# Kernel tuning notes

Hardware: AMD Instinct MI355X
Metric: run time of the kernel (lower is better)

The kernel has to match this reference:

```python
import jax, jax.numpy as jnp
import numpy as np

N, C = 131072, 32          # scene points, raw feature channels
K, L, B1 = 2048, 64, 8     # points per leaf, num leaves, level-1 branching
D_PROJ, D_HID, D = 128, 256, 512


def _lin(key, fan_in, fan_out):
    return jax.random.normal(key, (fan_in, fan_out), jnp.float32) / np.sqrt(fan_in)


def setup_inputs() -> dict:
    key = jax.random.key(0)
    ks = jax.random.split(key, 12)
    coords = jax.random.normal(ks[0], (N, 3), jnp.float32)
    feats = jax.random.normal(ks[1], (N, C), jnp.float32)
    # regular partition of the scene into 64 leaves of 2048 points each
    leaf_indices = jnp.arange(N, dtype=jnp.int32).reshape(L, K)
    leaf_center_idx = jax.random.randint(ks[2], (L,), 0, N, dtype=jnp.int32)
    l1_center_idx = jax.random.randint(ks[3], (B1,), 0, N, dtype=jnp.int32)
    return {
        'coords': coords, 'feats': feats,
        'leaf_indices': leaf_indices,
        'leaf_center_idx': leaf_center_idx,
        'l1_center_idx': l1_center_idx,
        'root_center_idx': 0,
        # projection MLP: C -> 128 -> 128
        'Wp1': _lin(ks[4], C, D_PROJ), 'bp1': jnp.zeros((D_PROJ,), jnp.float32),
        'Wp2': _lin(ks[5], D_PROJ, D_PROJ), 'bp2': jnp.zeros((D_PROJ,), jnp.float32),
        # encoder per-point MLP: (3 + 128) -> 256 -> 512
        'We1': _lin(ks[6], 3 + D_PROJ, D_HID), 'be1': jnp.zeros((D_HID,), jnp.float32),
        'We2': _lin(ks[7], D_HID, D), 'be2': jnp.zeros((D,), jnp.float32),
        # aggregator: (D + 3) -> 512 per child, max-pool, 512 -> 512
        'Wa1': _lin(ks[8], D + 3, D), 'ba1': jnp.zeros((D,), jnp.float32),
        'Wa2': _lin(ks[9], D, D), 'ba2': jnp.zeros((D,), jnp.float32),
    }


def reference(coords, feats, leaf_indices, leaf_center_idx, l1_center_idx,
              root_center_idx, Wp1, bp1, Wp2, bp2, We1, be1, We2, be2,
              Wa1, ba1, Wa2, ba2):
    # ---- leaves: gather + projection + PointNet encoder (batched over all leaves) ----
    pts = coords[leaf_indices]                       # (L, K, 3)
    pf = feats[leaf_indices]                         # (L, K, C)
    centers = coords[leaf_center_idx]                # (L, 3)
    rel = pts - centers[:, None, :]                  # relative coords
    proj = jax.nn.relu(pf @ Wp1 + bp1) @ Wp2 + bp2   # (L, K, D_PROJ)
    x = jnp.concatenate([rel, proj], axis=-1)        # (L, K, 3+D_PROJ)
    h = jax.nn.relu(x @ We1 + be1)                   # (L, K, D_HID)
    point_feats = jax.nn.relu(h @ We2 + be2)         # (L, K, D)
    leaf_feat = point_feats.max(axis=1)              # (L, D) max pool per leaf

    # ---- aggregator with spatial context ----
    def aggregate(child_feats, child_pos, parent_pos):
        r = child_pos - parent_pos[None, :]                       # (M, 3)
        z = jnp.concatenate([child_feats, r], axis=-1)            # (M, D+3)
        g = jax.nn.relu(z @ Wa1 + ba1)                            # (M, D)
        return g.max(axis=0) @ Wa2 + ba2                          # (D,)

    # level 1: each of B1 parents aggregates L//B1 leaf children
    cf = leaf_feat.reshape(B1, L // B1, D)
    cp = centers.reshape(B1, L // B1, 3)
    pp = coords[l1_center_idx]                                    # (B1, 3)
    level1 = jax.vmap(aggregate)(cf, cp, pp)                      # (B1, D)

    # level 0: root aggregates the B1 level-1 features
    root = aggregate(level1, pp, coords[root_center_idx])         # (D,)

    # rows: [level_0 (1), level_1 (B1), level_2 (L)]
    return jnp.concatenate([root[None, :], level1, leaf_feat], axis=0)
```

## Files before the change

### kernel.cpp

```cpp
#include <hip/hip_runtime.h>

#define NPTS   131072
#define CIN    32
#define KPL    2048
#define NLEAF  64
#define NB1    8
#define DPJ    128
#define DHID   256
#define DOUT   512
#define TM     128

typedef __attribute__((ext_vector_type(8))) short  short8;
typedef __attribute__((ext_vector_type(4))) float  f32x4;

__device__ __forceinline__ unsigned short f2bf(float x) {
    unsigned u = __float_as_uint(x);
    u += 0x7FFFu + ((u >> 16) & 1u);
    return (unsigned short)(u >> 16);
}

__global__ __launch_bounds__(256) void prep_weights(
    const float* __restrict__ Wp1, const float* __restrict__ We2,
    const float* __restrict__ Wp2, const float* __restrict__ We1,
    const float* __restrict__ bp2, const float* __restrict__ be1,
    unsigned short* __restrict__ wp1t, unsigned short* __restrict__ we2t,
    unsigned short* __restrict__ wft, float* __restrict__ bfused)
{
    const int b = blockIdx.x;
    if (b < 528) {
        int idx = b * 256 + threadIdx.x;
        if (idx < 4096) {
            int n = idx / 32, k = idx % 32;
            wp1t[idx] = f2bf(Wp1[k * DPJ + n]);
        } else if (idx < 4096 + 131072) {
            int i = idx - 4096;
            int n = i / 256, k = i % 256;
            we2t[i] = f2bf(We2[k * DOUT + n]);
        }
    } else if (b < 656) {
        const int k = b - 528;
        const int n = threadIdx.x;
        float a0 = 0.f, a1 = 0.f, a2 = 0.f, a3 = 0.f;
        #pragma unroll
        for (int j = 0; j < DPJ; j += 4) {
            a0 += Wp2[k * DPJ + j    ] * We1[(3 + j) * DHID + n];
            a1 += Wp2[k * DPJ + j + 1] * We1[(4 + j) * DHID + n];
            a2 += Wp2[k * DPJ + j + 2] * We1[(5 + j) * DHID + n];
            a3 += Wp2[k * DPJ + j + 3] * We1[(6 + j) * DHID + n];
        }
        wft[n * DPJ + k] = f2bf((a0 + a1) + (a2 + a3));
    } else {
        const int n = threadIdx.x;
        float s0 = be1[n], s1 = 0.f, s2 = 0.f, s3 = 0.f;
        #pragma unroll
        for (int j = 0; j < DPJ; j += 4) {
            s0 += bp2[j    ] * We1[(3 + j) * DHID + n];
            s1 += bp2[j + 1] * We1[(4 + j) * DHID + n];
            s2 += bp2[j + 2] * We1[(5 + j) * DHID + n];
            s3 += bp2[j + 3] * We1[(6 + j) * DHID + n];
        }
        bfused[n] = (s0 + s1) + (s2 + s3);
    }
}

template<int MF, int NF, int KSTEPS, int SB, int WK>
__device__ __forceinline__ void gemm_core(
    const char* sIn, const unsigned short* __restrict__ wt,
    const float* __restrict__ bias, int cb, int lr, int lg, f32x4 acc[MF][NF])
{
    #pragma unroll
    for (int n = 0; n < NF; ++n) {
        float bv = bias[cb + 16 * n + lr];
        #pragma unroll
        for (int m = 0; m < MF; ++m) acc[m][n] = f32x4{bv, bv, bv, bv};
    }
    #pragma unroll
    for (int kk = 0; kk < KSTEPS; ++kk) {
        short8 b[NF];
        #pragma unroll
        for (int n = 0; n < NF; ++n)
            b[n] = *reinterpret_cast<const short8*>(
                wt + (size_t)(cb + 16 * n + lr) * WK + kk * 32 + lg * 8);
        #pragma unroll
        for (int m = 0; m < MF; ++m) {
            int row  = 16 * m + lr;
            int byte = (row * SB + kk * 64 + lg * 16) ^ ((row & 7) << 4);
            short8 a = *reinterpret_cast<const short8*>(sIn + byte);
            #pragma unroll
            for (int n = 0; n < NF; ++n)
                acc[m][n] = __builtin_amdgcn_mfma_f32_16x16x32_bf16(a, b[n], acc[m][n], 0, 0, 0);
        }
    }
}

template<int MF, int NF, int SB, bool RELU>
__device__ __forceinline__ void store_frag(char* sOut, int cb, int lr, int lg, f32x4 acc[MF][NF])
{
    #pragma unroll
    for (int m = 0; m < MF; ++m) {
        #pragma unroll
        for (int r = 0; r < 4; ++r) {
            int row = 16 * m + lg * 4 + r;
            int rb  = row * SB;
            int sw  = (row & 7) << 4;
            #pragma unroll
            for (int n = 0; n < NF; ++n) {
                float v = acc[m][n][r];
                if (RELU) v = fmaxf(v, 0.f);
                int byte = (rb + (cb + 16 * n + lr) * 2) ^ sw;
                *reinterpret_cast<unsigned short*>(sOut + byte) = f2bf(v);
            }
        }
    }
}

template<int MF, int NF>
__device__ __forceinline__ void pool_frag(float* dst, int cb, int lr, int lg, f32x4 acc[MF][NF])
{
    #pragma unroll
    for (int n = 0; n < NF; ++n) {
        float vm = 0.f;
        #pragma unroll
        for (int m = 0; m < MF; ++m) {
            #pragma unroll
            for (int r = 0; r < 4; ++r) vm = fmaxf(vm, acc[m][n][r]);
        }
        vm = fmaxf(vm, __shfl_xor(vm, 16));
        vm = fmaxf(vm, __shfl_xor(vm, 32));
        if (lg == 0)
            atomicMax(reinterpret_cast<int*>(dst + cb + 16 * n + lr),
                      __float_as_int(vm));
    }
}

__global__ __launch_bounds__(256, 1) void leaf_mfma_kernel(
    const float* __restrict__ coords, const float* __restrict__ feats,
    const int* __restrict__ leaf_indices, const int* __restrict__ leaf_center_idx,
    const unsigned short* __restrict__ wp1t, const float* __restrict__ bp1,
    const unsigned short* __restrict__ wft, const float* __restrict__ bfused,
    const float* __restrict__ We1raw,
    const unsigned short* __restrict__ we2t, const float* __restrict__ be2,
    float* __restrict__ leaf_out)
{
    __shared__ __align__(16) char buf[96 * 1024];
    __shared__ float s_rel[TM][4];
    __shared__ float s_we1rel[3 * DHID];

    const int t    = threadIdx.x;
    const int lane = t & 63;
    const int w    = t >> 6;
    const int lr   = lane & 15;
    const int lg   = lane >> 4;

    const int l     = blockIdx.x >> 4;
    const int chunk = blockIdx.x & 15;
    const int base  = l * KPL + chunk * TM;

    char* const sX  = buf;
    char* const sH  = buf;
    char* const sP1 = buf + 65536;

    {
        const int p  = t >> 1;
        const int kq = (t & 1) << 4;
        const int gi = leaf_indices[base + p];
        const float* src = feats + (size_t)gi * CIN + kq;
        float4 v0 = *reinterpret_cast<const float4*>(src);
        float4 v1 = *reinterpret_cast<const float4*>(src + 4);
        float4 v2 = *reinterpret_cast<const float4*>(src + 8);
        float4 v3 = *reinterpret_cast<const float4*>(src + 12);
        short8 o0, o1;
        o0[0] = (short)f2bf(v0.x); o0[1] = (short)f2bf(v0.y);
        o0[2] = (short)f2bf(v0.z); o0[3] = (short)f2bf(v0.w);
        o0[4] = (short)f2bf(v1.x); o0[5] = (short)f2bf(v1.y);
        o0[6] = (short)f2bf(v1.z); o0[7] = (short)f2bf(v1.w);
        o1[0] = (short)f2bf(v2.x); o1[1] = (short)f2bf(v2.y);
        o1[2] = (short)f2bf(v2.z); o1[3] = (short)f2bf(v2.w);
        o1[4] = (short)f2bf(v3.x); o1[5] = (short)f2bf(v3.y);
        o1[6] = (short)f2bf(v3.z); o1[7] = (short)f2bf(v3.w);
        const int sw = (p & 7) << 4;
        int b0 = (p * (CIN * 2) + kq * 2) ^ sw;
        int b1 = (p * (CIN * 2) + kq * 2 + 16) ^ sw;
        *reinterpret_cast<short8*>(sX + b0) = o0;
        *reinterpret_cast<short8*>(sX + b1) = o1;
    }
    if (t < TM) {
        const int gi = leaf_indices[base + t];
        const int ci = leaf_center_idx[l];
        s_rel[t][0] = coords[gi * 3 + 0] - coords[ci * 3 + 0];
        s_rel[t][1] = coords[gi * 3 + 1] - coords[ci * 3 + 1];
        s_rel[t][2] = coords[gi * 3 + 2] - coords[ci * 3 + 2];
    }
    #pragma unroll
    for (int j = 0; j < 3; ++j) s_we1rel[j * DHID + t] = We1raw[j * DHID + t];
    __syncthreads();

    {
        f32x4 acc[8][2];
        gemm_core<8, 2, 1, CIN * 2, 32>(sX, wp1t, bp1, w * 32, lr, lg, acc);
        store_frag<8, 2, DPJ * 2, true>(sP1, w * 32, lr, lg, acc);
    }
    __syncthreads();

    {
        const int cb = w * 64;
        f32x4 acc[8][4];
        gemm_core<8, 4, 4, DPJ * 2, DPJ>(sP1, wft, bfused, cb, lr, lg, acc);
        #pragma unroll
        for (int m = 0; m < 8; ++m) {
            #pragma unroll
            for (int r = 0; r < 4; ++r) {
                int row = 16 * m + lg * 4 + r;
                float r0 = s_rel[row][0], r1 = s_rel[row][1], r2 = s_rel[row][2];
                #pragma unroll
                for (int n = 0; n < 4; ++n) {
                    int col = cb + 16 * n + lr;
                    acc[m][n][r] += r0 * s_we1rel[col]
                                  + r1 * s_we1rel[DHID + col]
                                  + r2 * s_we1rel[2 * DHID + col];
                }
            }
        }
        store_frag<8, 4, DHID * 2, true>(sH, cb, lr, lg, acc);
    }
    __syncthreads();

    {
        float* const dst = leaf_out + (size_t)l * DOUT;
        #pragma unroll
        for (int p4 = 0; p4 < 2; ++p4) {
            const int cb = w * 128 + p4 * 64;
            f32x4 acc[8][4];
            gemm_core<8, 4, 8, DHID * 2, 256>(sH, we2t, be2, cb, lr, lg, acc);
            pool_frag<8, 4>(dst, cb, lr, lg, acc);
        }
    }
}

__global__ __launch_bounds__(256) void agg_pool_kernel(
    const float* __restrict__ child,
    const float* __restrict__ coords,
    const int* __restrict__ child_idx,
    const int* __restrict__ parent_idx,
    const float* __restrict__ Wa1, const float* __restrict__ ba1,
    float* __restrict__ pooled)
{
    __shared__ float s_z[NB1][516];
    __shared__ float s_red[4][NB1][64];

    const int t  = threadIdx.x;
    const int b  = blockIdx.x;
    const int p  = b >> 3, cc = b & 7;
    const int c  = t & 63;
    const int col = cc * 64 + c;
    const int ks = t >> 6;

    {
        const int m = t >> 5, tt = t & 31;
        const float* src = child + (size_t)(p * NB1 + m) * DOUT;
        #pragma unroll
        for (int i = 0; i < 4; ++i) {
            const int idx = (i * 32 + tt) * 4;
            *reinterpret_cast<float4*>(&s_z[m][idx]) =
                *reinterpret_cast<const float4*>(src + idx);
        }
    }
    if (t < 24) {
        const int m = t / 3, j = t % 3;
        s_z[m][512 + j] = coords[child_idx[p * NB1 + m] * 3 + j]
                        - coords[parent_idx[p] * 3 + j];
    }
    __syncthreads();

    float acc[NB1] = {0.f, 0.f, 0.f, 0.f, 0.f, 0.f, 0.f, 0.f};
    const int k0 = ks * 128;
    #pragma unroll 32
    for (int i = 0; i < 128; ++i) {
        const int k = k0 + i;
        const float wv = Wa1[(size_t)k * DOUT + col];
        #pragma unroll
        for (int m = 0; m < NB1; ++m) acc[m] += s_z[m][k] * wv;
    }
    if (ks == 3) {
        #pragma unroll
        for (int k = 512; k < 515; ++k) {
            const float wv = Wa1[(size_t)k * DOUT + col];
            #pragma unroll
            for (int m = 0; m < NB1; ++m) acc[m] += s_z[m][k] * wv;
        }
    }
    #pragma unroll
    for (int m = 0; m < NB1; ++m) s_red[ks][m][c] = acc[m];
    __syncthreads();

    if (t < 64) {
        const float bv = ba1[col];
        float pm = 0.f;
        #pragma unroll
        for (int m = 0; m < NB1; ++m) {
            float v = bv + s_red[0][m][c] + s_red[1][m][c]
                         + s_red[2][m][c] + s_red[3][m][c];
            pm = fmaxf(pm, v);
        }
        pooled[(size_t)p * DOUT + col] = pm;
    }
}

__global__ __launch_bounds__(256) void agg_out_kernel(
    const float* __restrict__ pooled,
    const float* __restrict__ Wa2, const float* __restrict__ ba2,
    float* __restrict__ outbase)
{
    __shared__ float s_p[DOUT];
    __shared__ float s_red[4][64];

    const int t  = threadIdx.x;
    const int b  = blockIdx.x;
    const int p  = b >> 3, cc = b & 7;
    const int c  = t & 63;
    const int col = cc * 64 + c;
    const int ks = t >> 6;

    if (t < 128)
        *reinterpret_cast<float4*>(&s_p[t * 4]) =
            *reinterpret_cast<const float4*>(pooled + (size_t)p * DOUT + t * 4);
    __syncthreads();

    float acc = 0.f;
    const int k0 = ks * 128;
    #pragma unroll 32
    for (int i = 0; i < 128; ++i) {
        const int k = k0 + i;
        acc += s_p[k] * Wa2[(size_t)k * DOUT + col];
    }
    s_red[ks][c] = acc;
    __syncthreads();

    if (t < 64)
        outbase[(size_t)p * DOUT + col] =
            ba2[col] + s_red[0][c] + s_red[1][c] + s_red[2][c] + s_red[3][c];
}

extern "C" void kernel_launch(void* const* d_in, const int* in_sizes, int n_in,
                              void* d_out, int out_size, void* d_ws, size_t ws_size,
                              hipStream_t stream)
{
    const float* coords          = (const float*)d_in[0];
    const float* feats           = (const float*)d_in[1];
    const int*   leaf_indices    = (const int*)d_in[2];
    const int*   leaf_center_idx = (const int*)d_in[3];
    const int*   l1_center_idx   = (const int*)d_in[4];
    const int*   root_center_idx = (const int*)d_in[5];
    const float* Wp1 = (const float*)d_in[6];
    const float* bp1 = (const float*)d_in[7];
    const float* Wp2 = (const float*)d_in[8];
    const float* bp2 = (const float*)d_in[9];
    const float* We1 = (const float*)d_in[10];
    const float* be1 = (const float*)d_in[11];
    const float* We2 = (const float*)d_in[12];
    const float* be2 = (const float*)d_in[13];
    const float* Wa1 = (const float*)d_in[14];
    const float* ba1 = (const float*)d_in[15];
    const float* Wa2 = (const float*)d_in[16];
    const float* ba2 = (const float*)d_in[17];

    float* out = (float*)d_out;
    char*  ws  = (char*)d_ws;
    unsigned short* wp1t     = (unsigned short*)ws;
    unsigned short* we2t     = (unsigned short*)(ws + 8192);
    unsigned short* wft      = (unsigned short*)(ws + 270336);
    float*          bfused   = (float*)(ws + 335872);
    float*          pooledL1 = (float*)(ws + 336896);
    float*          pooledR  = (float*)(ws + 353280);

    hipMemsetAsync(out + (size_t)(1 + NB1) * DOUT, 0,
                   (size_t)NLEAF * DOUT * sizeof(float), stream);

    prep_weights<<<dim3(657), dim3(256), 0, stream>>>(
        Wp1, We2, Wp2, We1, bp2, be1, wp1t, we2t, wft, bfused);

    leaf_mfma_kernel<<<dim3(NLEAF * (KPL / TM)), dim3(256), 0, stream>>>(
        coords, feats, leaf_indices, leaf_center_idx,
        wp1t, bp1, wft, bfused, We1, we2t, be2,
        out + (size_t)(1 + NB1) * DOUT);

    agg_pool_kernel<<<dim3(NB1 * 8), dim3(256), 0, stream>>>(
        out + (size_t)(1 + NB1) * DOUT, coords, leaf_center_idx, l1_center_idx,
        Wa1, ba1, pooledL1);
    agg_out_kernel<<<dim3(NB1 * 8), dim3(256), 0, stream>>>(
        pooledL1, Wa2, ba2, out + DOUT);

    agg_pool_kernel<<<dim3(8), dim3(256), 0, stream>>>(
        out + DOUT, coords, l1_center_idx, root_center_idx,
        Wa1, ba1, pooledR);
    agg_out_kernel<<<dim3(8), dim3(256), 0, stream>>>(
        pooledR, Wa2, ba2, out);
}
```

Measured before the change: 114.2 us.

## Fuse aggregator levels into one kernel with atomic-counter inter-block dependencies

Replaces the four small aggregator launches with a single 144-block kernel. Blocks wait on global atomic counters (spin-wait with s_sleep) for their producer stage before running, and read cross-block data through atomic loads to bypass stale caches. The leaf-row memset and counter reset are folded into extra blocks of the weight-prep kernel. This removes several launch gaps and one memset call, but relies on all 144 blocks being co-resident and adds spin-wait and atomic-read overhead.

```diff
diff --git a/kernel.cpp b/kernel.cpp
--- a/kernel.cpp
+++ b/kernel.cpp
@@ -24,7 +24,8 @@
     const float* __restrict__ Wp2, const float* __restrict__ We1,
     const float* __restrict__ bp2, const float* __restrict__ be1,
     unsigned short* __restrict__ wp1t, unsigned short* __restrict__ we2t,
-    unsigned short* __restrict__ wft, float* __restrict__ bfused)
+    unsigned short* __restrict__ wft, float* __restrict__ bfused,
+    float* __restrict__ leaf_rows, unsigned* __restrict__ cnts)
 {
     const int b = blockIdx.x;
     if (b < 528) {
@@ -49,7 +50,7 @@
             a3 += Wp2[k * DPJ + j + 3] * We1[(6 + j) * DHID + n];
         }
         wft[n * DPJ + k] = f2bf((a0 + a1) + (a2 + a3));
-    } else {
+    } else if (b == 656) {
         const int n = threadIdx.x;
         float s0 = be1[n], s1 = 0.f, s2 = 0.f, s3 = 0.f;
         #pragma unroll
@@ -60,6 +61,11 @@
             s3 += bp2[j + 3] * We1[(6 + j) * DHID + n];
         }
         bfused[n] = (s0 + s1) + (s2 + s3);
+    } else if (b < 689) {
+        int i = (b - 657) * 256 + threadIdx.x;
+        reinterpret_cast<float4*>(leaf_rows)[i] = float4{0.f, 0.f, 0.f, 0.f};
+    } else {
+        if (threadIdx.x < 10) cnts[threadIdx.x] = 0u;
     }
 }
 
@@ -237,38 +243,50 @@
     }
 }
 
-__global__ __launch_bounds__(256) void agg_pool_kernel(
-    const float* __restrict__ child,
-    const float* __restrict__ coords,
-    const int* __restrict__ child_idx,
-    const int* __restrict__ parent_idx,
-    const float* __restrict__ Wa1, const float* __restrict__ ba1,
-    float* __restrict__ pooled)
-{
-    __shared__ float s_z[NB1][516];
-    __shared__ float s_red[4][NB1][64];
-
+__device__ __forceinline__ void spin_wait(unsigned* cnt, unsigned target) {
+    if (threadIdx.x == 0) {
+        while (atomicAdd(cnt, 0u) < target) __builtin_amdgcn_s_sleep(8);
+        __threadfence();
+    }
+    __syncthreads();
+}
+__device__ __forceinline__ void signal(unsigned* cnt) {
+    __syncthreads();
+    if (threadIdx.x == 0) { __threadfence(); atomicAdd(cnt, 1u); }
+}
+
+template<bool ATOMIC>
+__device__ __forceinline__ void do_pool(
+    const float* child, const float* coords, const int* child_idx, int parent,
+    const float* Wa1, const float* ba1, float* pooled_row, int cc,
+    float (*s_z)[516], float (*s_red)[NB1][64])
+{
     const int t  = threadIdx.x;
-    const int b  = blockIdx.x;
-    const int p  = b >> 3, cc = b & 7;
     const int c  = t & 63;
     const int col = cc * 64 + c;
     const int ks = t >> 6;
 
     {
         const int m = t >> 5, tt = t & 31;
-        const float* src = child + (size_t)(p * NB1 + m) * DOUT;
-        #pragma unroll
-        for (int i = 0; i < 4; ++i) {
-            const int idx = (i * 32 + tt) * 4;
-            *reinterpret_cast<float4*>(&s_z[m][idx]) =
-                *reinterpret_cast<const float4*>(src + idx);
+        const float* src = child + (size_t)m * DOUT;
+        if (ATOMIC) {
+            #pragma unroll
+            for (int i = 0; i < 16; ++i) {
+                int idx = tt + i * 32;
+                s_z[m][idx] = atomicAdd(const_cast<float*>(src) + idx, 0.f);
+            }
+        } else {
+            #pragma unroll
+            for (int i = 0; i < 4; ++i) {
+                const int idx = (i * 32 + tt) * 4;
+                *reinterpret_cast<float4*>(&s_z[m][idx]) =
+                    *reinterpret_cast<const float4*>(src + idx);
+            }
         }
     }
     if (t < 24) {
         const int m = t / 3, j = t % 3;
-        s_z[m][512 + j] = coords[child_idx[p * NB1 + m] * 3 + j]
-                        - coords[parent_idx[p] * 3 + j];
+        s_z[m][512 + j] = coords[child_idx[m] * 3 + j] - coords[parent * 3 + j];
     }
     __syncthreads();
 
@@ -302,28 +320,22 @@
                          + s_red[2][m][c] + s_red[3][m][c];
             pm = fmaxf(pm, v);
         }
-        pooled[(size_t)p * DOUT + col] = pm;
-    }
-}
-
-__global__ __launch_bounds__(256) void agg_out_kernel(
-    const float* __restrict__ pooled,
-    const float* __restrict__ Wa2, const float* __restrict__ ba2,
-    float* __restrict__ outbase)
-{
-    __shared__ float s_p[DOUT];
-    __shared__ float s_red[4][64];
-
+        pooled_row[col] = pm;
+    }
+    __syncthreads();
+}
+
+__device__ __forceinline__ void do_out(
+    const float* pooled_row, const float* Wa2, const float* ba2,
+    float* out_row, int cc, float* s_p, float (*s_red2)[64])
+{
     const int t  = threadIdx.x;
-    const int b  = blockIdx.x;
-    const int p  = b >> 3, cc = b & 7;
     const int c  = t & 63;
     const int col = cc * 64 + c;
     const int ks = t >> 6;
 
-    if (t < 128)
-        *reinterpret_cast<float4*>(&s_p[t * 4]) =
-            *reinterpret_cast<const float4*>(pooled + (size_t)p * DOUT + t * 4);
+    s_p[t * 2]     = atomicAdd(const_cast<float*>(pooled_row) + t * 2, 0.f);
+    s_p[t * 2 + 1] = atomicAdd(const_cast<float*>(pooled_row) + t * 2 + 1, 0.f);
     __syncthreads();
 
     float acc = 0.f;
@@ -333,12 +345,57 @@
         const int k = k0 + i;
         acc += s_p[k] * Wa2[(size_t)k * DOUT + col];
     }
-    s_red[ks][c] = acc;
+    s_red2[ks][c] = acc;
     __syncthreads();
 
     if (t < 64)
-        outbase[(size_t)p * DOUT + col] =
-            ba2[col] + s_red[0][c] + s_red[1][c] + s_red[2][c] + s_red[3][c];
+        out_row[col] = ba2[col] + s_red2[0][c] + s_red2[1][c]
+                                + s_red2[2][c] + s_red2[3][c];
+    __syncthreads();
+}
+
+__global__ __launch_bounds__(256) void agg_fused(
+    const float* __restrict__ coords,
+    const int* __restrict__ leaf_center_idx,
+    const int* __restrict__ l1_center_idx,
+    const int* __restrict__ root_center_idx,
+    const float* __restrict__ Wa1, const float* __restrict__ ba1,
+    const float* __restrict__ Wa2, const float* __restrict__ ba2,
+    float* __restrict__ out,
+    float* __restrict__ pooledL1, float* __restrict__ pooledR,
+    unsigned* __restrict__ cnts)
+{
+    __shared__ float s_z[NB1][516];
+    __shared__ float s_red[4][NB1][64];
+    __shared__ float s_p[DOUT];
+    __shared__ float s_red2[4][64];
+
+    const int b = blockIdx.x;
+    float* const leaf_rows = out + (size_t)(1 + NB1) * DOUT;
+
+    if (b < 64) {
+        const int p = b >> 3, cc = b & 7;
+        do_pool<false>(leaf_rows + (size_t)p * NB1 * DOUT, coords,
+                       leaf_center_idx + p * NB1, l1_center_idx[p],
+                       Wa1, ba1, pooledL1 + (size_t)p * DOUT, cc, s_z, s_red);
+        signal(&cnts[p]);
+    } else if (b < 128) {
+        const int i = b - 64, p = i >> 3, cc = i & 7;
+        spin_wait(&cnts[p], 8u);
+        do_out(pooledL1 + (size_t)p * DOUT, Wa2, ba2,
+               out + (size_t)(1 + p) * DOUT, cc, s_p, s_red2);
+        signal(&cnts[8]);
+    } else if (b < 136) {
+        const int cc = b - 128;
+        spin_wait(&cnts[8], 64u);
+        do_pool<true>(out + DOUT, coords, l1_center_idx, root_center_idx[0],
+                      Wa1, ba1, pooledR, cc, s_z, s_red);
+        signal(&cnts[9]);
+    } else {
+        const int cc = b - 136;
+        spin_wait(&cnts[9], 8u);
+        do_out(pooledR, Wa2, ba2, out, cc, s_p, s_red2);
+    }
 }
 
 extern "C" void kernel_launch(void* const* d_in, const int* in_sizes, int n_in,
@@ -372,27 +429,18 @@
     float*          bfused   = (float*)(ws + 335872);
     float*          pooledL1 = (float*)(ws + 336896);
     float*          pooledR  = (float*)(ws + 353280);
-
-    hipMemsetAsync(out + (size_t)(1 + NB1) * DOUT, 0,
-                   (size_t)NLEAF * DOUT * sizeof(float), stream);
-
-    prep_weights<<<dim3(657), dim3(256), 0, stream>>>(
-        Wp1, We2, Wp2, We1, bp2, be1, wp1t, we2t, wft, bfused);
+    unsigned*       cnts     = (unsigned*)(ws + 355328);
+
+    prep_weights<<<dim3(690), dim3(256), 0, stream>>>(
+        Wp1, We2, Wp2, We1, bp2, be1, wp1t, we2t, wft, bfused,
+        out + (size_t)(1 + NB1) * DOUT, cnts);
 
     leaf_mfma_kernel<<<dim3(NLEAF * (KPL / TM)), dim3(256), 0, stream>>>(
         coords, feats, leaf_indices, leaf_center_idx,
         wp1t, bp1, wft, bfused, We1, we2t, be2,
         out + (size_t)(1 + NB1) * DOUT);
 
-    agg_pool_kernel<<<dim3(NB1 * 8), dim3(256), 0, stream>>>(
-        out + (size_t)(1 + NB1) * DOUT, coords, leaf_center_idx, l1_center_idx,
-        Wa1, ba1, pooledL1);
-    agg_out_kernel<<<dim3(NB1 * 8), dim3(256), 0, stream>>>(
-        pooledL1, Wa2, ba2, out + DOUT);
-
-    agg_pool_kernel<<<dim3(8), dim3(256), 0, stream>>>(
-        out + DOUT, coords, l1_center_idx, root_center_idx,
-        Wa1, ba1, pooledR);
-    agg_out_kernel<<<dim3(8), dim3(256), 0, stream>>>(
-        pooledR, Wa2, ba2, out);
-}
+    agg_fused<<<dim3(144), dim3(256), 0, stream>>>(
+        coords, leaf_center_idx, l1_center_idx, root_center_idx,
+        Wa1, ba1, Wa2, ba2, out, pooledL1, pooledR, cnts);
+}
```

New measurement: 141.5 us. 23.9% more time.
